# Kernel tuning notes

Hardware: AMD Instinct MI355X
Metric: run time of the kernel (lower is better)

Reference implementation:

```python
import jax, jax.numpy as jnp
import numpy as np

EMB = 16
L = 100
B = 8192
BN_EPS = 1e-5


def _bn(x, g, b):
    # BatchNorm1d in training mode: biased batch stats over dim 0. x: [b, EMB]
    mu = jnp.mean(x, axis=0)
    var = jnp.mean((x - mu) ** 2, axis=0)
    return g * (x - mu) / jnp.sqrt(var + BN_EPS) + b


def _pool(me, aw, g6, b6, a6):
    # me: [b, L, EMB] masked embeddings; aw: [b, L, 1] masked attention logits
    s = jnp.sum(me, axis=1)                       # sum pool
    mean = jnp.mean(me, axis=1)                   # mean over full L (incl. padding), as in torch
    sq = me * me
    l2 = jnp.sum(sq, axis=-1)                     # [b, L]
    mx_i = jnp.argmax(l2, axis=1)                 # first max, matches torch.max
    mn_i = jnp.argmin(jnp.where(l2 == 0, jnp.asarray(9999.0, l2.dtype), l2), axis=1)
    mx = jnp.take_along_axis(me, mx_i[:, None, None], axis=1)[:, 0]
    mn = jnp.take_along_axis(me, mn_i[:, None, None], axis=1)[:, 0]
    attw = jax.nn.softmax(aw, axis=1)             # softmax over L incl. zeroed pads (faithful)
    at = jnp.sum(me * attw, axis=1)
    ko = 0.5 * (s * s - jnp.sum(sq, axis=1))      # korder (FM-style)
    ko = ko / jnp.maximum(jnp.linalg.norm(ko, axis=-1, keepdims=True), 1e-12)
    # branch order: sum, mean, max, min, korder, atten (matches torch.cat order)
    pools = jnp.stack([
        _bn(s, g6[0], b6[0]), _bn(mean, g6[1], b6[1]), _bn(mx, g6[2], b6[2]),
        _bn(mn, g6[3], b6[3]), _bn(ko, g6[4], b6[4]), _bn(at, g6[5], b6[5])], axis=1)
    w = jax.nn.softmax(a6)[None, :, None]
    return jnp.sum(pools * w, axis=1)             # [b, EMB]


def setup_inputs() -> dict:
    key = jax.random.key(0)
    ks = jax.random.split(key, 24)
    f32 = jnp.float32
    inp = {
        'uid': jax.random.randint(ks[0], (B,), 0, 139000),
        'mid': jax.random.randint(ks[1], (B,), 0, 132000),
        'yr': jax.random.randint(ks[2], (B,), 0, 150),
        'ids_ug': jax.random.randint(ks[3], (B, L), 0, 30),
        'ids_urb': jax.random.randint(ks[4], (B, L), 0, 132000),
        'ids_mg': jax.random.randint(ks[5], (B, L), 0, 30),
        'ids_mt': jax.random.randint(ks[6], (B, L), 0, 41000),
        'len_ug': jax.random.randint(ks[7], (B,), 1, L + 1),
        'len_urb': jax.random.randint(ks[8], (B,), 1, L + 1),
        'len_mg': jax.random.randint(ks[9], (B,), 1, L + 1),
        'len_mt': jax.random.randint(ks[10], (B,), 1, L + 1),
        'emb_userId': jax.random.normal(ks[11], (139000, EMB), f32) * 0.05,
        'emb_movieId': jax.random.normal(ks[12], (132000, EMB), f32) * 0.05,
        'emb_tagId': jax.random.normal(ks[13], (41000, EMB), f32) * 0.05,
        'emb_genreId': jax.random.normal(ks[14], (30, EMB), f32) * 0.05,
        'emb_year': jax.random.normal(ks[15], (150, EMB), f32) * 0.05,
        # init_param(): atten embeddings ~ N(1.0, 1e-6)
        'att_movieId': 1.0 + jax.random.normal(ks[16], (132000, 1), f32) * 1e-6,
        'att_tagId': 1.0 + jax.random.normal(ks[17], (41000, 1), f32) * 1e-6,
        'att_genreId': 1.0 + jax.random.normal(ks[18], (30, 1), f32) * 1e-6,
        'bn_gamma': jnp.ones((4, 6, EMB), f32),
        'bn_beta': jnp.zeros((4, 6, EMB), f32),
        'alpha': jnp.ones((4, 6), f32),
        'W1': jax.random.normal(ks[19], (112, 64), f32) * 0.05,
        'b1': jnp.zeros((64,), f32),
        'W2': jax.random.normal(ks[20], (64, 32), f32) * 0.05,
        'b2': jnp.zeros((32,), f32),
        'W3': jax.random.normal(ks[21], (32, 1), f32) * 0.05,
        'b3': jnp.zeros((1,), f32),
    }
    return inp


def reference(uid, mid, yr, ids_ug, ids_urb, ids_mg, ids_mt,
              len_ug, len_urb, len_mg, len_mt,
              emb_userId, emb_movieId, emb_tagId, emb_genreId, emb_year,
              att_movieId, att_tagId, att_genreId,
              bn_gamma, bn_beta, alpha, W1, b1, W2, b2, W3, b3):
    emb1 = jnp.concatenate([emb_userId[uid], emb_movieId[mid], emb_year[yr]], axis=1)  # [b, 48]
    ar = jnp.arange(L)
    fields = [
        (ids_ug, len_ug, emb_genreId, att_genreId),
        (ids_urb, len_urb, emb_movieId, att_movieId),
        (ids_mg, len_mg, emb_genreId, att_genreId),
        (ids_mt, len_mt, emb_tagId, att_tagId),
    ]
    pooled = []
    for i, (ids, ln, tab, atab) in enumerate(fields):
        m = (ln[:, None] > ar)[..., None].astype(tab.dtype)  # [b, L, 1]
        me = tab[ids] * m
        aw = atab[ids] * m
        pooled.append(_pool(me, aw, bn_gamma[i], bn_beta[i], alpha[i]))
    x = jnp.concatenate([emb1] + pooled, axis=1)  # [b, 112]
    h = jax.nn.relu(x @ W1 + b1)
    h = jax.nn.relu(h @ W2 + b2)
    return jax.nn.sigmoid(h @ W3 + b3)[:, 0]
```

## Files before the change

### kernel.cpp

```cpp
#include <hip/hip_runtime.h>
#include <math.h>

#define BATCH 8192
#define L 100
#define EMB 16
#define NCH 384

#define POOLED_FLOATS (4 * BATCH * 96)
#define POOLED_BYTES  (POOLED_FLOATS * 4)

__global__ __launch_bounds__(256) void pool_kernel(
    const int* __restrict__ ids_ug, const int* __restrict__ ids_urb,
    const int* __restrict__ ids_mg, const int* __restrict__ ids_mt,
    const int* __restrict__ len_ug, const int* __restrict__ len_urb,
    const int* __restrict__ len_mg, const int* __restrict__ len_mt,
    const float* __restrict__ emb_movie, const float* __restrict__ emb_tag,
    const float* __restrict__ emb_genre,
    const float* __restrict__ att_movie, const float* __restrict__ att_tag,
    const float* __restrict__ att_genre,
    float* __restrict__ pooled, double* __restrict__ sums, double* __restrict__ sumsqs)
{
    const int f = blockIdx.y;
    const int* ids; const int* lens; const float* tab; const float* atab;
    switch (f) {
        case 0: ids = ids_ug;  lens = len_ug;  tab = emb_genre; atab = att_genre; break;
        case 1: ids = ids_urb; lens = len_urb; tab = emb_movie; atab = att_movie; break;
        case 2: ids = ids_mg;  lens = len_mg;  tab = emb_genre; atab = att_genre; break;
        default:ids = ids_mt;  lens = len_mt;  tab = emb_tag;   atab = att_tag;   break;
    }
    const int tid = threadIdx.x;
    const int sub = tid >> 4;
    const int j   = (tid >> 2) & 3;
    const int c   = tid & 3;
    const int b   = blockIdx.x * 16 + sub;
    const int ln  = lens[b];

    const int* idrow = ids + (size_t)b * L;
    const float4* __restrict__ tab4 = (const float4*)tab;

    float4 s   = make_float4(0.f, 0.f, 0.f, 0.f);
    float4 ssq = s, att = s, mxv = s, mnv = s;
    float expsum = 0.f;
    float bestmx = -1e30f; int lx = 0x7fffffff;
    float bestmn =  1e30f; int lm = 0x7fffffff;

    int l  = j;
    int id = (l < ln) ? idrow[l] : 0;
    while (l < ln) {
        const int nl  = l + 4;
        const int nid = (nl < ln) ? idrow[nl] : 0;
        const float4 v = tab4[(size_t)id * 4 + c];
        const float aw = atab[id];
        float4 v2;
        v2.x = v.x * v.x; v2.y = v.y * v.y; v2.z = v.z * v.z; v2.w = v.w * v.w;
        s.x += v.x; s.y += v.y; s.z += v.z; s.w += v.w;
        ssq.x += v2.x; ssq.y += v2.y; ssq.z += v2.z; ssq.w += v2.w;
        float pl2 = (v2.x + v2.y) + (v2.z + v2.w);
        float l2 = pl2 + __shfl_xor(pl2, 1);
        l2 += __shfl_xor(l2, 2);
        if (l2 > bestmx) { bestmx = l2; lx = l; mxv = v; }
        float l2m = (l2 == 0.0f) ? 9999.0f : l2;
        if (l2m < bestmn) { bestmn = l2m; lm = l; mnv = v; }
        float ew = __expf(aw);
        expsum += ew;
        att.x += v.x * ew; att.y += v.y * ew; att.z += v.z * ew; att.w += v.w * ew;
        l = nl; id = nid;
    }

    #pragma unroll
    for (int m = 4; m <= 8; m <<= 1) {
        float obx = __shfl_xor(bestmx, m);
        int   olx = __shfl_xor(lx, m);
        float ax = __shfl_xor(mxv.x, m), ay = __shfl_xor(mxv.y, m);
        float az = __shfl_xor(mxv.z, m), aw2 = __shfl_xor(mxv.w, m);
        if (obx > bestmx || (obx == bestmx && olx < lx)) {
            bestmx = obx; lx = olx; mxv = make_float4(ax, ay, az, aw2);
        }
        float obn = __shfl_xor(bestmn, m);
        int   olm = __shfl_xor(lm, m);
        float bx = __shfl_xor(mnv.x, m), by = __shfl_xor(mnv.y, m);
        float bz = __shfl_xor(mnv.z, m), bw = __shfl_xor(mnv.w, m);
        if (obn < bestmn || (obn == bestmn && olm < lm)) {
            bestmn = obn; lm = olm; mnv = make_float4(bx, by, bz, bw);
        }
        s.x += __shfl_xor(s.x, m); s.y += __shfl_xor(s.y, m);
        s.z += __shfl_xor(s.z, m); s.w += __shfl_xor(s.w, m);
        ssq.x += __shfl_xor(ssq.x, m); ssq.y += __shfl_xor(ssq.y, m);
        ssq.z += __shfl_xor(ssq.z, m); ssq.w += __shfl_xor(ssq.w, m);
        att.x += __shfl_xor(att.x, m); att.y += __shfl_xor(att.y, m);
        att.z += __shfl_xor(att.z, m); att.w += __shfl_xor(att.w, m);
        expsum += __shfl_xor(expsum, m);
    }
    expsum += (float)(L - ln);

    float4 mean;
    mean.x = s.x * (1.0f / L); mean.y = s.y * (1.0f / L);
    mean.z = s.z * (1.0f / L); mean.w = s.w * (1.0f / L);
    float4 ko;
    ko.x = 0.5f * (s.x * s.x - ssq.x); ko.y = 0.5f * (s.y * s.y - ssq.y);
    ko.z = 0.5f * (s.z * s.z - ssq.z); ko.w = 0.5f * (s.w * s.w - ssq.w);
    float pk = (ko.x * ko.x + ko.y * ko.y) + (ko.z * ko.z + ko.w * ko.w);
    float kn2 = pk + __shfl_xor(pk, 1);
    kn2 += __shfl_xor(kn2, 2);
    float rn = 1.0f / fmaxf(sqrtf(kn2), 1e-12f);
    ko.x *= rn; ko.y *= rn; ko.z *= rn; ko.w *= rn;
    float ie = 1.0f / expsum;
    att.x *= ie; att.y *= ie; att.z *= ie; att.w *= ie;

    float4 pv[6] = { s, mean, mxv, mnv, ko, att };

    __shared__ float tile[16][100];
    float4* prow = (float4*)(pooled + ((size_t)(f * BATCH + b)) * 96);
    if (j == 0) {
        #pragma unroll
        for (int p = 0; p < 6; ++p) {
            prow[p * 4 + c] = pv[p];
            *(float4*)&tile[sub][p * 16 + c * 4] = pv[p];
        }
    }
    __syncthreads();
    if (tid < 96) {
        float sm = 0.f, sq = 0.f;
        #pragma unroll
        for (int s2 = 0; s2 < 16; ++s2) {
            float x = tile[s2][tid];
            sm += x;
            sq += x * x;
        }
        atomicAdd(&sums[f * 96 + tid],   (double)sm);
        atomicAdd(&sumsqs[f * 96 + tid], (double)sq);
    }
}

__global__ __launch_bounds__(384) void coef_kernel(
    const double* __restrict__ sums, const double* __restrict__ sumsqs,
    const float* __restrict__ gamma, const float* __restrict__ beta,
    const float* __restrict__ alpha,
    float* __restrict__ coefA, float* __restrict__ coefB)
{
    int c = threadIdx.x;
    if (c >= NCH) return;
    int f = c / 96;
    int p = (c % 96) >> 4;
    double mu  = sums[c]   * (1.0 / BATCH);
    double var = sumsqs[c] * (1.0 / BATCH) - mu * mu;
    float inv = (float)(1.0 / sqrt(var + 1e-5));
    float g  = gamma[c];
    float bb = beta[c];
    float amax = -1e30f;
    for (int q = 0; q < 6; ++q) amax = fmaxf(amax, alpha[f * 6 + q]);
    float wsum = 0.f;
    for (int q = 0; q < 6; ++q) wsum += __expf(alpha[f * 6 + q] - amax);
    float wp = __expf(alpha[f * 6 + p] - amax) / wsum;
    float muf = (float)mu;
    coefA[c] = wp * g * inv;
    coefB[c] = wp * (bb - g * muf * inv);
}

#define SPB 16
__global__ __launch_bounds__(256) void final_kernel(
    const int* __restrict__ uid, const int* __restrict__ mid, const int* __restrict__ yr,
    const float* __restrict__ emb_user, const float* __restrict__ emb_movie,
    const float* __restrict__ emb_year,
    const float* __restrict__ pooled,
    const float* __restrict__ coefA, const float* __restrict__ coefB,
    const float* __restrict__ W1, const float* __restrict__ b1,
    const float* __restrict__ W2, const float* __restrict__ b2,
    const float* __restrict__ W3, const float* __restrict__ b3,
    float* __restrict__ out)
{
    __shared__ float sW1[112 * 64];
    __shared__ float sW2[64 * 32];
    __shared__ float sW3[32];
    __shared__ float sb1[64];
    __shared__ float sb2[32];
    __shared__ float xt[SPB][112];
    __shared__ float h1t[SPB][64];

    const int tid = threadIdx.x;
    for (int i = tid; i < 112 * 16; i += 256)
        ((float4*)sW1)[i] = ((const float4*)W1)[i];
    for (int i = tid; i < 64 * 8; i += 256)
        ((float4*)sW2)[i] = ((const float4*)W2)[i];
    if (tid < 32) sW3[tid] = W3[tid];
    if (tid < 64) sb1[tid] = b1[tid];
    if (tid < 32) sb2[tid] = b2[tid];

    const int sub = tid >> 4;
    const int e   = tid & 15;
    const int b   = blockIdx.x * SPB + sub;

    xt[sub][e]      = emb_user [(size_t)uid[b] * EMB + e];
    xt[sub][16 + e] = emb_movie[(size_t)mid[b] * EMB + e];
    xt[sub][32 + e] = emb_year [(size_t)yr[b]  * EMB + e];

    #pragma unroll
    for (int f = 0; f < 4; ++f) {
        const float* pr = pooled + ((size_t)(f * BATCH + b)) * 96;
        float acc = 0.f;
        #pragma unroll
        for (int p = 0; p < 6; ++p) {
            int c = f * 96 + p * 16 + e;
            acc += coefA[c] * pr[p * 16 + e] + coefB[c];
        }
        xt[sub][48 + f * 16 + e] = acc;
    }
    __syncthreads();

    float4 h1 = ((float4*)sb1)[e];
    for (int k = 0; k < 112; ++k) {
        float xk = xt[sub][k];
        float4 w = ((float4*)sW1)[k * 16 + e];
        h1.x += xk * w.x; h1.y += xk * w.y; h1.z += xk * w.z; h1.w += xk * w.w;
    }
    float4 h1r;
    h1r.x = fmaxf(h1.x, 0.f); h1r.y = fmaxf(h1.y, 0.f);
    h1r.z = fmaxf(h1.z, 0.f); h1r.w = fmaxf(h1.w, 0.f);
    *(float4*)&h1t[sub][e * 4] = h1r;
    __syncthreads();

    float2 h2 = ((float2*)sb2)[e];
    for (int k = 0; k < 64; ++k) {
        float hk = h1t[sub][k];
        float2 w = ((float2*)sW2)[k * 16 + e];
        h2.x += hk * w.x; h2.y += hk * w.y;
    }
    float part = fmaxf(h2.x, 0.f) * sW3[2 * e] + fmaxf(h2.y, 0.f) * sW3[2 * e + 1];
    part += __shfl_xor(part, 1);
    part += __shfl_xor(part, 2);
    part += __shfl_xor(part, 4);
    part += __shfl_xor(part, 8);
    if (e == 0) {
        float t = part + b3[0];
        out[b] = 1.f / (1.f + __expf(-t));
    }
}

extern "C" void kernel_launch(void* const* d_in, const int* in_sizes, int n_in,
                              void* d_out, int out_size, void* d_ws, size_t ws_size,
                              hipStream_t stream) {
    const int* uid     = (const int*)d_in[0];
    const int* mid     = (const int*)d_in[1];
    const int* yr      = (const int*)d_in[2];
    const int* ids_ug  = (const int*)d_in[3];
    const int* ids_urb = (const int*)d_in[4];
    const int* ids_mg  = (const int*)d_in[5];
    const int* ids_mt  = (const int*)d_in[6];
    const int* len_ug  = (const int*)d_in[7];
    const int* len_urb = (const int*)d_in[8];
    const int* len_mg  = (const int*)d_in[9];
    const int* len_mt  = (const int*)d_in[10];
    const float* emb_user  = (const float*)d_in[11];
    const float* emb_movie = (const float*)d_in[12];
    const float* emb_tag   = (const float*)d_in[13];
    const float* emb_genre = (const float*)d_in[14];
    const float* emb_year  = (const float*)d_in[15];
    const float* att_movie = (const float*)d_in[16];
    const float* att_tag   = (const float*)d_in[17];
    const float* att_genre = (const float*)d_in[18];
    const float* bn_gamma  = (const float*)d_in[19];
    const float* bn_beta   = (const float*)d_in[20];
    const float* alpha     = (const float*)d_in[21];
    const float* W1 = (const float*)d_in[22];
    const float* b1 = (const float*)d_in[23];
    const float* W2 = (const float*)d_in[24];
    const float* b2 = (const float*)d_in[25];
    const float* W3 = (const float*)d_in[26];
    const float* b3 = (const float*)d_in[27];
    float* out = (float*)d_out;

    float*  pooled = (float*)d_ws;
    double* sums   = (double*)((char*)d_ws + POOLED_BYTES);
    double* sumsqs = sums + NCH;
    float*  coefA  = (float*)(sums + 2 * NCH);
    float*  coefB  = coefA + NCH;

    hipMemsetAsync(sums, 0, 2 * NCH * sizeof(double), stream);
    pool_kernel<<<dim3(BATCH / 16, 4), 256, 0, stream>>>(
        ids_ug, ids_urb, ids_mg, ids_mt,
        len_ug, len_urb, len_mg, len_mt,
        emb_movie, emb_tag, emb_genre,
        att_movie, att_tag, att_genre,
        pooled, sums, sumsqs);
    coef_kernel<<<1, 384, 0, stream>>>(sums, sumsqs, bn_gamma, bn_beta, alpha,
                                       coefA, coefB);
    final_kernel<<<BATCH / SPB, 256, 0, stream>>>(
        uid, mid, yr, emb_user, emb_movie, emb_year,
        pooled, coefA, coefB, W1, b1, W2, b2, W3, b3, out);
}
```

Before: 172.5 us.

## Defer argmax/argmin to shared-memory pass and unroll gather loop by two

The main gather loop now processes two sequence positions per iteration and no longer tracks the running max/min vectors. Per-position half L2 norms go to a shared buffer, and a second pass over all 16 lanes finds the first argmax and argmin. The winning rows are then re-gathered from the embedding table. This cuts per-iteration shuffles and branch work and adds memory-level parallelism, at the cost of a 12.8KB shared buffer, extra barriers and two extra gathers per row.

```diff
diff --git a/kernel.cpp b/kernel.cpp
--- a/kernel.cpp
+++ b/kernel.cpp
@@ -30,59 +30,85 @@
     }
     const int tid = threadIdx.x;
     const int sub = tid >> 4;
-    const int j   = (tid >> 2) & 3;
-    const int c   = tid & 3;
+    const int e   = tid & 15;
+    const int j   = e >> 2;
+    const int c   = e & 3;
     const int b   = blockIdx.x * 16 + sub;
     const int ln  = lens[b];
 
     const int* idrow = ids + (size_t)b * L;
     const float4* __restrict__ tab4 = (const float4*)tab;
 
+    __shared__ float l2buf[16][100][2];
+
     float4 s   = make_float4(0.f, 0.f, 0.f, 0.f);
-    float4 ssq = s, att = s, mxv = s, mnv = s;
+    float4 ssq = s, att = s;
     float expsum = 0.f;
-    float bestmx = -1e30f; int lx = 0x7fffffff;
-    float bestmn =  1e30f; int lm = 0x7fffffff;
-
-    int l  = j;
-    int id = (l < ln) ? idrow[l] : 0;
-    while (l < ln) {
-        const int nl  = l + 4;
-        const int nid = (nl < ln) ? idrow[nl] : 0;
-        const float4 v = tab4[(size_t)id * 4 + c];
-        const float aw = atab[id];
-        float4 v2;
-        v2.x = v.x * v.x; v2.y = v.y * v.y; v2.z = v.z * v.z; v2.w = v.w * v.w;
-        s.x += v.x; s.y += v.y; s.z += v.z; s.w += v.w;
-        ssq.x += v2.x; ssq.y += v2.y; ssq.z += v2.z; ssq.w += v2.w;
-        float pl2 = (v2.x + v2.y) + (v2.z + v2.w);
-        float l2 = pl2 + __shfl_xor(pl2, 1);
-        l2 += __shfl_xor(l2, 2);
-        if (l2 > bestmx) { bestmx = l2; lx = l; mxv = v; }
+
+    int l = j;
+    for (; l + 4 < ln; l += 8) {
+        const int id0 = idrow[l];
+        const int id1 = idrow[l + 4];
+        const float4 v0 = tab4[(size_t)id0 * 4 + c];
+        const float4 v1 = tab4[(size_t)id1 * 4 + c];
+        const float aw0 = atab[id0];
+        const float aw1 = atab[id1];
+        float4 w0, w1;
+        w0.x = v0.x * v0.x; w0.y = v0.y * v0.y; w0.z = v0.z * v0.z; w0.w = v0.w * v0.w;
+        w1.x = v1.x * v1.x; w1.y = v1.y * v1.y; w1.z = v1.z * v1.z; w1.w = v1.w * v1.w;
+        s.x += v0.x + v1.x; s.y += v0.y + v1.y; s.z += v0.z + v1.z; s.w += v0.w + v1.w;
+        ssq.x += w0.x + w1.x; ssq.y += w0.y + w1.y;
+        ssq.z += w0.z + w1.z; ssq.w += w0.w + w1.w;
+        float p0 = (w0.x + w0.y) + (w0.z + w0.w);
+        float p1 = (w1.x + w1.y) + (w1.z + w1.w);
+        p0 += __shfl_xor(p0, 1);
+        p1 += __shfl_xor(p1, 1);
+        l2buf[sub][l][c >> 1]     = p0;
+        l2buf[sub][l + 4][c >> 1] = p1;
+        const float e0 = __expf(aw0);
+        const float e1 = __expf(aw1);
+        expsum += e0 + e1;
+        att.x += v0.x * e0 + v1.x * e1; att.y += v0.y * e0 + v1.y * e1;
+        att.z += v0.z * e0 + v1.z * e1; att.w += v0.w * e0 + v1.w * e1;
+    }
+    if (l < ln) {
+        const int id0 = idrow[l];
+        const float4 v0 = tab4[(size_t)id0 * 4 + c];
+        const float aw0 = atab[id0];
+        float4 w0;
+        w0.x = v0.x * v0.x; w0.y = v0.y * v0.y; w0.z = v0.z * v0.z; w0.w = v0.w * v0.w;
+        s.x += v0.x; s.y += v0.y; s.z += v0.z; s.w += v0.w;
+        ssq.x += w0.x; ssq.y += w0.y; ssq.z += w0.z; ssq.w += w0.w;
+        float p0 = (w0.x + w0.y) + (w0.z + w0.w);
+        p0 += __shfl_xor(p0, 1);
+        l2buf[sub][l][c >> 1] = p0;
+        const float e0 = __expf(aw0);
+        expsum += e0;
+        att.x += v0.x * e0; att.y += v0.y * e0; att.z += v0.z * e0; att.w += v0.w * e0;
+    }
+    __syncthreads();
+
+    float bmx = -1e30f; int lx = 0x7fffffff;
+    float bmn =  1e30f; int lm = 0x7fffffff;
+    for (int q = e; q < ln; q += 16) {
+        float2 t = *(float2*)&l2buf[sub][q][0];
+        float l2 = t.x + t.y;
+        if (l2 > bmx) { bmx = l2; lx = q; }
         float l2m = (l2 == 0.0f) ? 9999.0f : l2;
-        if (l2m < bestmn) { bestmn = l2m; lm = l; mnv = v; }
-        float ew = __expf(aw);
-        expsum += ew;
-        att.x += v.x * ew; att.y += v.y * ew; att.z += v.z * ew; att.w += v.w * ew;
-        l = nl; id = nid;
+        if (l2m < bmn) { bmn = l2m; lm = q; }
+    }
+    #pragma unroll
+    for (int m = 1; m <= 8; m <<= 1) {
+        float o  = __shfl_xor(bmx, m);
+        int   ol = __shfl_xor(lx, m);
+        if (o > bmx || (o == bmx && ol < lx)) { bmx = o; lx = ol; }
+        float on  = __shfl_xor(bmn, m);
+        int   onl = __shfl_xor(lm, m);
+        if (on < bmn || (on == bmn && onl < lm)) { bmn = on; lm = onl; }
     }
 
     #pragma unroll
     for (int m = 4; m <= 8; m <<= 1) {
-        float obx = __shfl_xor(bestmx, m);
-        int   olx = __shfl_xor(lx, m);
-        float ax = __shfl_xor(mxv.x, m), ay = __shfl_xor(mxv.y, m);
-        float az = __shfl_xor(mxv.z, m), aw2 = __shfl_xor(mxv.w, m);
-        if (obx > bestmx || (obx == bestmx && olx < lx)) {
-            bestmx = obx; lx = olx; mxv = make_float4(ax, ay, az, aw2);
-        }
-        float obn = __shfl_xor(bestmn, m);
-        int   olm = __shfl_xor(lm, m);
-        float bx = __shfl_xor(mnv.x, m), by = __shfl_xor(mnv.y, m);
-        float bz = __shfl_xor(mnv.z, m), bw = __shfl_xor(mnv.w, m);
-        if (obn < bestmn || (obn == bestmn && olm < lm)) {
-            bestmn = obn; lm = olm; mnv = make_float4(bx, by, bz, bw);
-        }
         s.x += __shfl_xor(s.x, m); s.y += __shfl_xor(s.y, m);
         s.z += __shfl_xor(s.z, m); s.w += __shfl_xor(s.w, m);
         ssq.x += __shfl_xor(ssq.x, m); ssq.y += __shfl_xor(ssq.y, m);
@@ -107,15 +133,22 @@
     float ie = 1.0f / expsum;
     att.x *= ie; att.y *= ie; att.z *= ie; att.w *= ie;
 
-    float4 pv[6] = { s, mean, mxv, mnv, ko, att };
-
-    __shared__ float tile[16][100];
-    float4* prow = (float4*)(pooled + ((size_t)(f * BATCH + b)) * 96);
-    if (j == 0) {
+    float4 mxv = make_float4(0.f, 0.f, 0.f, 0.f), mnv = mxv;
+    if (e < 4) {
+        mxv = tab4[(size_t)idrow[lx] * 4 + e];
+        mnv = tab4[(size_t)idrow[lm] * 4 + e];
+    }
+
+    __syncthreads();
+    float* tile = (float*)l2buf;
+
+    if (e < 4) {
+        float4 pv[6] = { s, mean, mxv, mnv, ko, att };
+        float4* prow = (float4*)(pooled + ((size_t)(f * BATCH + b)) * 96);
         #pragma unroll
         for (int p = 0; p < 6; ++p) {
-            prow[p * 4 + c] = pv[p];
-            *(float4*)&tile[sub][p * 16 + c * 4] = pv[p];
+            prow[p * 4 + e] = pv[p];
+            *(float4*)&tile[sub * 100 + p * 16 + e * 4] = pv[p];
         }
     }
     __syncthreads();
@@ -123,7 +156,7 @@
         float sm = 0.f, sq = 0.f;
         #pragma unroll
         for (int s2 = 0; s2 < 16; ++s2) {
-            float x = tile[s2][tid];
+            float x = tile[s2 * 100 + tid];
             sm += x;
             sq += x * x;
         }
```

Result: slower. 177.1 us (+2.6%).
